# Performance work log

Measured on AMD Instinct MI355X. Metric: run time of the kernel, lower is better.

Reference implementation:

```python
import jax, jax.numpy as jnp
import numpy as np

I, J, B, H = 256, 256, 64, 1024
NHID, NCLS = 1024, 3


def setup_inputs() -> dict:
    key = jax.random.key(0)
    ks = jax.random.split(key, 12)
    inp = {
        "P_enc": jax.random.normal(ks[0], (I, B, H), jnp.float32),
        "H_enc": jax.random.normal(ks[1], (J, B, H), jnp.float32),
        "P_emb": jax.random.normal(ks[2], (I, B, H), jnp.float32),
        "H_emb": jax.random.normal(ks[3], (J, B, H), jnp.float32),
        "prem_mask": jax.random.bernoulli(ks[4], 0.15, (I, B)),
        "hypo_mask": jax.random.bernoulli(ks[5], 0.15, (J, B)),
        # compare MLP: Linear(2H, NHID) -> ReLU -> Linear(NHID, NHID) -> ReLU
        "cW1": jax.random.normal(ks[6], (2 * H, NHID), jnp.float32) * 0.02,
        "cb1": jnp.zeros((NHID,), jnp.float32),
        "cW2": jax.random.normal(ks[7], (NHID, NHID), jnp.float32) * 0.02,
        "cb2": jnp.zeros((NHID,), jnp.float32),
        # agg MLP: Linear(2*NHID, NHID) -> ReLU -> Linear(NHID, NCLS)
        "aW1": jax.random.normal(ks[8], (2 * NHID, NHID), jnp.float32) * 0.02,
        "ab1": jnp.zeros((NHID,), jnp.float32),
        "aW2": jax.random.normal(ks[9], (NHID, NCLS), jnp.float32) * 0.02,
        "ab2": jnp.zeros((NCLS,), jnp.float32),
    }
    return inp


def reference(P_enc, H_enc, P_emb, H_emb, prem_mask, hypo_mask,
              cW1, cb1, cW2, cb2, aW1, ab1, aW2, ab2):
    # Dropout is identity at inference.
    def compare(x):
        h = jax.nn.relu(x @ cW1 + cb1)
        return jax.nn.relu(h @ cW2 + cb2)

    # S[b,i,j] = <P_enc[i,b,:], H_enc[j,b,:]>
    S = jnp.einsum('ibh,jbh->bij', P_enc, H_enc)

    # Premise-side masking on rows i, softmax over premise positions (axis=1)
    S_m = jnp.where(prem_mask.T[:, :, None], -jnp.inf, S)  # [b,i,j]
    P_attn = jax.nn.softmax(S_m, axis=1)
    H_ctx = jnp.einsum('bij,ibh->jbh', P_attn, P_emb)      # [j,b,h]
    H_ctx = jnp.where(hypo_mask[:, :, None], 0.0, H_ctx)
    H_comp = compare(jnp.concatenate([H_emb, H_ctx], axis=-1))  # [j,b,nhid]

    # Hypothesis-side: transpose of the UNMASKED scores
    St = jnp.swapaxes(S, 1, 2)                              # [b,j,i]
    St = jnp.where(hypo_mask.T[:, :, None], -jnp.inf, St)
    H_attn = jax.nn.softmax(St, axis=1)
    P_ctx = jnp.einsum('bji,jbh->ibh', H_attn, H_emb)       # [i,b,h]
    P_ctx = jnp.where(prem_mask[:, :, None], 0.0, P_ctx)
    P_comp = compare(jnp.concatenate([P_emb, P_ctx], axis=-1))  # [i,b,nhid]

    pool = jnp.concatenate([H_comp.sum(axis=0), P_comp.sum(axis=0)], axis=-1)  # [b, 2*nhid]
    out = jax.nn.relu(pool @ aW1 + ab1) @ aW2 + ab2          # [b, ncls]
    return out
```

## Files before the change

### kernel.cpp

```cpp
#include <hip/hip_runtime.h>
#include <cstdint>
#include <cstddef>

typedef unsigned short ushort_t;
typedef unsigned char uchar_t;
typedef __attribute__((ext_vector_type(4))) float f4;
typedef __attribute__((ext_vector_type(4))) unsigned int u4;

#define DEVI static __device__ __forceinline__

DEVI ushort_t f2bf(float x) {
  union { float f; unsigned int u; } v; v.f = x;
  unsigned int r = v.u + 0x7fffu + ((v.u >> 16) & 1u);
  return (ushort_t)(r >> 16);
}
DEVI float bf2f(ushort_t b) {
  union { unsigned int u; float f; } v; v.u = ((unsigned int)b) << 16;
  return v.f;
}
DEVI unsigned pk2(ushort_t a, ushort_t b) { return (unsigned)a | ((unsigned)b << 16); }

DEVI void mfma16(f4& c, u4 a, u4 b) {
  asm("v_mfma_f32_16x16x32_bf16 %0, %1, %2, %0" : "+v"(c) : "v"(a), "v"(b));
}

constexpr int LDR = 40;

__global__ __launch_bounds__(256) void prep_masks_kernel(
    const uchar_t* __restrict__ prem, const uchar_t* __restrict__ hypo,
    uchar_t* __restrict__ premT, uchar_t* __restrict__ hypoT) {
  __shared__ int flagP, flagH;
  int t = threadIdx.x;
  if (t == 0) { flagP = 0; flagH = 0; }
  __syncthreads();
  int locP = 0, locH = 0;
  for (int i = t; i < 16384; i += 256) {
    if (i & 3) { locP |= prem[i]; locH |= hypo[i]; }
  }
  if (locP) atomicOr(&flagP, 1);
  if (locH) atomicOr(&flagH, 1);
  __syncthreads();
  bool p8 = flagP != 0, h8 = flagH != 0;
  for (int i = t; i < 16384; i += 256) {
    int p = i >> 6, b = i & 63;
    premT[b * 256 + p] = p8 ? prem[i] : prem[i * 4];
    hypoT[b * 256 + p] = h8 ? hypo[i] : hypo[i * 4];
  }
}

__global__ __launch_bounds__(256) void transpose_w_kernel(
    const float* __restrict__ Win, ushort_t* __restrict__ Thi,
    ushort_t* __restrict__ Tlo, int N, int K) {
  __shared__ float tl[64][65];
  int k0 = blockIdx.x * 64, n0 = blockIdx.y * 64;
  int t = threadIdx.x;
#pragma unroll
  for (int it = 0; it < 16; ++it) {
    int idx = t + it * 256;
    int k = idx >> 6, n = idx & 63;
    tl[n][k] = Win[(size_t)(k0 + k) * N + n0 + n];
  }
  __syncthreads();
#pragma unroll
  for (int it = 0; it < 16; ++it) {
    int idx = t + it * 256;
    int n = idx >> 6, k = idx & 63;
    float x = tl[n][k];
    ushort_t h = f2bf(x);
    Thi[(size_t)(n0 + n) * K + k0 + k] = h;
    if (Tlo) Tlo[(size_t)(n0 + n) * K + k0 + k] = f2bf(x - bf2f(h));
  }
}

__global__ __launch_bounds__(256) void gemm_s_kernel(
    const float* __restrict__ Penc, const float* __restrict__ Henc,
    float* __restrict__ S) {
  __shared__ ushort_t lAh[128 * LDR], lAl[128 * LDR], lBh[128 * LDR], lBl[128 * LDR];
  const int t = threadIdx.x;
  const int b = blockIdx.z;
  const int i0 = blockIdx.x * 128, j0 = blockIdx.y * 128;
  const float* Ab = Penc + (size_t)i0 * 64 * 1024 + (size_t)b * 1024;
  const float* Bb = Henc + (size_t)j0 * 64 * 1024 + (size_t)b * 1024;
  const int lda = 64 * 1024;
  const int lane = t & 63, wave = t >> 6;
  const int wr = (wave >> 1) << 6, wc = (wave & 1) << 6;
  const int fr = lane & 15, fg = lane >> 4;

  f4 acc[4][4];
#pragma unroll
  for (int m = 0; m < 4; ++m)
#pragma unroll
    for (int n = 0; n < 4; ++n) acc[m][n] = f4{0.f, 0.f, 0.f, 0.f};

  for (int k0 = 0; k0 < 1024; k0 += 32) {
    __syncthreads();
#pragma unroll
    for (int c = 0; c < 2; ++c) {
      int ch = t + (c << 8);
      int row = ch >> 2, kp = (ch & 3) << 3;
      {
        const float* p = Ab + (size_t)row * lda + k0 + kp;
        f4 x0 = *(const f4*)p, x1 = *(const f4*)(p + 4);
        ushort_t hh[8], ll[8];
#pragma unroll
        for (int q = 0; q < 4; ++q) {
          ushort_t h0 = f2bf(x0[q]); hh[q] = h0; ll[q] = f2bf(x0[q] - bf2f(h0));
          ushort_t h1 = f2bf(x1[q]); hh[4 + q] = h1; ll[4 + q] = f2bf(x1[q] - bf2f(h1));
        }
        u4 hv = { pk2(hh[0], hh[1]), pk2(hh[2], hh[3]), pk2(hh[4], hh[5]), pk2(hh[6], hh[7]) };
        u4 lv = { pk2(ll[0], ll[1]), pk2(ll[2], ll[3]), pk2(ll[4], ll[5]), pk2(ll[6], ll[7]) };
        *(u4*)(lAh + row * LDR + kp) = hv;
        *(u4*)(lAl + row * LDR + kp) = lv;
      }
      {
        const float* p = Bb + (size_t)row * lda + k0 + kp;
        f4 x0 = *(const f4*)p, x1 = *(const f4*)(p + 4);
        ushort_t hh[8], ll[8];
#pragma unroll
        for (int q = 0; q < 4; ++q) {
          ushort_t h0 = f2bf(x0[q]); hh[q] = h0; ll[q] = f2bf(x0[q] - bf2f(h0));
          ushort_t h1 = f2bf(x1[q]); hh[4 + q] = h1; ll[4 + q] = f2bf(x1[q] - bf2f(h1));
        }
        u4 hv = { pk2(hh[0], hh[1]), pk2(hh[2], hh[3]), pk2(hh[4], hh[5]), pk2(hh[6], hh[7]) };
        u4 lv = { pk2(ll[0], ll[1]), pk2(ll[2], ll[3]), pk2(ll[4], ll[5]), pk2(ll[6], ll[7]) };
        *(u4*)(lBh + row * LDR + kp) = hv;
        *(u4*)(lBl + row * LDR + kp) = lv;
      }
    }
    __syncthreads();
    u4 ah[4], al[4], bh[4], bl[4];
#pragma unroll
    for (int m = 0; m < 4; ++m) {
      int off = (wr + m * 16 + fr) * LDR + (fg << 3);
      ah[m] = *(const u4*)(lAh + off);
      al[m] = *(const u4*)(lAl + off);
    }
#pragma unroll
    for (int n = 0; n < 4; ++n) {
      int off = (wc + n * 16 + fr) * LDR + (fg << 3);
      bh[n] = *(const u4*)(lBh + off);
      bl[n] = *(const u4*)(lBl + off);
    }
#pragma unroll
    for (int m = 0; m < 4; ++m)
#pragma unroll
      for (int n = 0; n < 4; ++n) {
        mfma16(acc[m][n], ah[m], bh[n]);
        mfma16(acc[m][n], ah[m], bl[n]);
        mfma16(acc[m][n], al[m], bh[n]);
      }
  }

  float* Sb = S + (size_t)b * 256 * 256;
#pragma unroll
  for (int m = 0; m < 4; ++m)
#pragma unroll
    for (int n = 0; n < 4; ++n)
#pragma unroll
      for (int r = 0; r < 4; ++r) {
        int row = i0 + wr + m * 16 + fg * 4 + r;
        int col = j0 + wc + n * 16 + fr;
        Sb[(size_t)row * 256 + col] = acc[m][n][r];
      }
}

__global__ __launch_bounds__(256) void softmax_rows_kernel(
    const float* __restrict__ S, const uchar_t* __restrict__ hypoT,
    ushort_t* __restrict__ W) {
  int r = blockIdx.x * 4 + (threadIdx.x >> 6);
  int lane = threadIdx.x & 63;
  int b = r >> 8;
  const float* row = S + (size_t)r * 256;
  f4 x = *(const f4*)(row + lane * 4);
  const uchar_t* mp = hypoT + b * 256 + lane * 4;
  float v0 = mp[0] ? -1e30f : x[0];
  float v1 = mp[1] ? -1e30f : x[1];
  float v2 = mp[2] ? -1e30f : x[2];
  float v3 = mp[3] ? -1e30f : x[3];
  float m = fmaxf(fmaxf(v0, v1), fmaxf(v2, v3));
#pragma unroll
  for (int off = 32; off > 0; off >>= 1) m = fmaxf(m, __shfl_xor(m, off));
  float e0 = expf(v0 - m), e1 = expf(v1 - m), e2 = expf(v2 - m), e3 = expf(v3 - m);
  float s = e0 + e1 + e2 + e3;
#pragma unroll
  for (int off = 32; off > 0; off >>= 1) s += __shfl_xor(s, off);
  float rinv = 1.0f / s;
  u4 dummy;
  (void)dummy;
  ushort_t w0 = f2bf(e0 * rinv), w1 = f2bf(e1 * rinv), w2 = f2bf(e2 * rinv), w3 = f2bf(e3 * rinv);
  unsigned out0 = pk2(w0, w1), out1 = pk2(w2, w3);
  typedef __attribute__((ext_vector_type(2))) unsigned int u2;
  *(u2*)(W + (size_t)r * 256 + lane * 4) = u2{out0, out1};
}

__global__ __launch_bounds__(256) void softmax_cols_kernel(
    const float* __restrict__ S, const uchar_t* __restrict__ premT,
    ushort_t* __restrict__ V) {
  __shared__ float tl[32][257];
  __shared__ float pm[8][32], ps[8][32], mfin[32], rs[32];
  int t = threadIdx.x;
  int jl = t & 31, ig = t >> 5;
  int b = blockIdx.y, j0 = blockIdx.x * 32;
  const float* Sb = S + (size_t)b * 65536;
  const uchar_t* pmsk = premT + b * 256;
  for (int i = ig; i < 256; i += 8)
    tl[jl][i] = pmsk[i] ? -1e30f : Sb[(size_t)i * 256 + j0 + jl];
  __syncthreads();
  float m = -3e30f;
#pragma unroll 8
  for (int ii = 0; ii < 32; ++ii) m = fmaxf(m, tl[jl][ig * 32 + ii]);
  float s = 0.f;
#pragma unroll 8
  for (int ii = 0; ii < 32; ++ii) s += expf(tl[jl][ig * 32 + ii] - m);
  pm[ig][jl] = m; ps[ig][jl] = s;
  __syncthreads();
  if (t < 32) {
    float M = pm[0][t];
#pragma unroll
    for (int g = 1; g < 8; ++g) M = fmaxf(M, pm[g][t]);
    float ss = 0.f;
#pragma unroll
    for (int g = 0; g < 8; ++g) ss += ps[g][t] * expf(pm[g][t] - M);
    mfin[t] = M; rs[t] = 1.0f / ss;
  }
  __syncthreads();
  for (int j2 = 0; j2 < 32; ++j2) {
    float val = expf(tl[j2][t] - mfin[j2]) * rs[j2];
    V[((size_t)b * 256 + j0 + j2) * 256 + t] = f2bf(val);
  }
}

__global__ __launch_bounds__(256) void transpose_pos_h_kernel(
    const float* __restrict__ E, ushort_t* __restrict__ T) {
  __shared__ ushort_t tl[64][65];
  int i0 = blockIdx.x * 64, h0 = blockIdx.y * 64, b = blockIdx.z;
  int t = threadIdx.x;
#pragma unroll
  for (int it = 0; it < 16; ++it) {
    int idx = t + it * 256;
    int i = idx >> 6, h = idx & 63;
    tl[h][i] = f2bf(E[((size_t)(i0 + i) * 64 + b) * 1024 + h0 + h]);
  }
  __syncthreads();
#pragma unroll
  for (int it = 0; it < 16; ++it) {
    int idx = t + it * 256;
    int h = idx >> 6, i = idx & 63;
    T[((size_t)b * 1024 + h0 + h) * 256 + i0 + i] = tl[h][i];
  }
}

__global__ __launch_bounds__(256) void cast_half_kernel(
    const float* __restrict__ E, ushort_t* __restrict__ X) {
  size_t idx = (size_t)blockIdx.x * 256 + threadIdx.x;
  size_t r = idx >> 7;
  int h8 = ((int)idx & 127) << 3;
  const f4* p = (const f4*)(E + r * 1024 + h8);
  f4 a = p[0], c = p[1];
  ushort_t hh[8];
#pragma unroll
  for (int q = 0; q < 4; ++q) { hh[q] = f2bf(a[q]); hh[4 + q] = f2bf(c[q]); }
  u4 v = { pk2(hh[0], hh[1]), pk2(hh[2], hh[3]), pk2(hh[4], hh[5]), pk2(hh[6], hh[7]) };
  *(u4*)(X + r * 2048 + h8) = v;
}

DEVI void gemm_core(const ushort_t* __restrict__ A, int lda,
                    const ushort_t* __restrict__ B, int ldb, int K,
                    ushort_t* lA, ushort_t* lB, f4 acc[4][4],
                    int t, int wr, int wc, int fr, int fg) {
  for (int k0 = 0; k0 < K; k0 += 32) {
    __syncthreads();
#pragma unroll
    for (int c = 0; c < 2; ++c) {
      int ch = t + (c << 8);
      int row = ch >> 2, kp = (ch & 3) << 3;
      *(u4*)(lA + row * LDR + kp) = *(const u4*)(A + (size_t)row * lda + k0 + kp);
      *(u4*)(lB + row * LDR + kp) = *(const u4*)(B + (size_t)row * ldb + k0 + kp);
    }
    __syncthreads();
    u4 af[4], bfr[4];
#pragma unroll
    for (int m = 0; m < 4; ++m) af[m] = *(const u4*)(lA + (wr + m * 16 + fr) * LDR + (fg << 3));
#pragma unroll
    for (int n = 0; n < 4; ++n) bfr[n] = *(const u4*)(lB + (wc + n * 16 + fr) * LDR + (fg << 3));
#pragma unroll
    for (int m = 0; m < 4; ++m)
#pragma unroll
      for (int n = 0; n < 4; ++n) mfma16(acc[m][n], af[m], bfr[n]);
  }
}

__global__ __launch_bounds__(256) void gemm_ctx_kernel(
    const ushort_t* __restrict__ Attn, const ushort_t* __restrict__ T,
    const uchar_t* __restrict__ maskT, ushort_t* __restrict__ X) {
  __shared__ ushort_t lA[128 * LDR], lB[128 * LDR];
  int t = threadIdx.x;
  int b = blockIdx.z;
  int m0 = blockIdx.x * 128, n0 = blockIdx.y * 128;
  const ushort_t* A = Attn + (size_t)b * 65536 + (size_t)m0 * 256;
  const ushort_t* B = T + (size_t)b * 1024 * 256 + (size_t)n0 * 256;
  int lane = t & 63, wave = t >> 6;
  int wr = (wave >> 1) << 6, wc = (wave & 1) << 6;
  int fr = lane & 15, fg = lane >> 4;
  f4 acc[4][4];
#pragma unroll
  for (int m = 0; m < 4; ++m)
#pragma unroll
    for (int n = 0; n < 4; ++n) acc[m][n] = f4{0.f, 0.f, 0.f, 0.f};
  gemm_core(A, 256, B, 256, 256, lA, lB, acc, t, wr, wc, fr, fg);
#pragma unroll
  for (int m = 0; m < 4; ++m)
#pragma unroll
    for (int n = 0; n < 4; ++n)
#pragma unroll
      for (int r = 0; r < 4; ++r) {
        int gm = m0 + wr + m * 16 + fg * 4 + r;
        int gn = n0 + wc + n * 16 + fr;
        float v = maskT[b * 256 + gm] ? 0.f : acc[m][n][r];
        X[((size_t)gm * 64 + b) * 2048 + 1024 + gn] = f2bf(v);
      }
}

__global__ __launch_bounds__(256) void gemm_mlp_kernel(
    const ushort_t* __restrict__ A, int lda, const ushort_t* __restrict__ W,
    const float* __restrict__ bias, ushort_t* __restrict__ C, int K) {
  __shared__ ushort_t lA[128 * LDR], lB[128 * LDR];
  int t = threadIdx.x;
  int m0 = blockIdx.x * 128, n0 = blockIdx.y * 128;
  int lane = t & 63, wave = t >> 6;
  int wr = (wave >> 1) << 6, wc = (wave & 1) << 6;
  int fr = lane & 15, fg = lane >> 4;
  f4 acc[4][4];
#pragma unroll
  for (int m = 0; m < 4; ++m)
#pragma unroll
    for (int n = 0; n < 4; ++n) acc[m][n] = f4{0.f, 0.f, 0.f, 0.f};
  gemm_core(A + (size_t)m0 * lda, lda, W + (size_t)n0 * K, K, K, lA, lB, acc,
            t, wr, wc, fr, fg);
#pragma unroll
  for (int m = 0; m < 4; ++m)
#pragma unroll
    for (int n = 0; n < 4; ++n)
#pragma unroll
      for (int r = 0; r < 4; ++r) {
        int gm = m0 + wr + m * 16 + fg * 4 + r;
        int gn = n0 + wc + n * 16 + fr;
        float v = acc[m][n][r] + bias[gn];
        v = v > 0.f ? v : 0.f;
        C[(size_t)gm * 1024 + gn] = f2bf(v);
      }
}

__global__ __launch_bounds__(256) void pool_reduce_kernel(
    const ushort_t* __restrict__ H2, float* __restrict__ pool, int coff) {
  int n = blockIdx.x * 256 + threadIdx.x;
  int b = blockIdx.y;
  float s = 0.f;
  for (int j = 0; j < 256; ++j)
    s += bf2f(H2[((size_t)j * 64 + b) * 1024 + n]);
  pool[b * 2048 + coff + n] = s;
}

__global__ __launch_bounds__(256) void pool_split_kernel(
    const float* __restrict__ pool, ushort_t* __restrict__ ph, ushort_t* __restrict__ pl) {
  int i = blockIdx.x * 256 + threadIdx.x;
  float x = pool[i];
  ushort_t h = f2bf(x);
  ph[i] = h;
  pl[i] = f2bf(x - bf2f(h));
}

__global__ __launch_bounds__(256) void gemm_agg1_kernel(
    const ushort_t* __restrict__ Ph, const ushort_t* __restrict__ Pl,
    const ushort_t* __restrict__ Wh, const ushort_t* __restrict__ Wl,
    const float* __restrict__ bias, float* __restrict__ z) {
  __shared__ ushort_t lAh[64 * LDR], lAl[64 * LDR], lBh[128 * LDR], lBl[128 * LDR];
  int t = threadIdx.x;
  int n0 = blockIdx.x * 128;
  int lane = t & 63, wave = t >> 6;
  int wc = wave * 32;
  int fr = lane & 15, fg = lane >> 4;
  f4 acc[4][2];
#pragma unroll
  for (int m = 0; m < 4; ++m)
#pragma unroll
    for (int n = 0; n < 2; ++n) acc[m][n] = f4{0.f, 0.f, 0.f, 0.f};

  for (int k0 = 0; k0 < 2048; k0 += 32) {
    __syncthreads();
    {
      int row = t >> 2, kp = (t & 3) << 3;
      *(u4*)(lAh + row * LDR + kp) = *(const u4*)(Ph + (size_t)row * 2048 + k0 + kp);
      *(u4*)(lAl + row * LDR + kp) = *(const u4*)(Pl + (size_t)row * 2048 + k0 + kp);
    }
#pragma unroll
    for (int c = 0; c < 2; ++c) {
      int ch = t + (c << 8);
      int row = ch >> 2, kp = (ch & 3) << 3;
      *(u4*)(lBh + row * LDR + kp) = *(const u4*)(Wh + (size_t)(n0 + row) * 2048 + k0 + kp);
      *(u4*)(lBl + row * LDR + kp) = *(const u4*)(Wl + (size_t)(n0 + row) * 2048 + k0 + kp);
    }
    __syncthreads();
    u4 ah[4], al[4], bh[2], bl[2];
#pragma unroll
    for (int m = 0; m < 4; ++m) {
      int off = (m * 16 + fr) * LDR + (fg << 3);
      ah[m] = *(const u4*)(lAh + off);
      al[m] = *(const u4*)(lAl + off);
    }
#pragma unroll
    for (int n = 0; n < 2; ++n) {
      int off = (wc + n * 16 + fr) * LDR + (fg << 3);
      bh[n] = *(const u4*)(lBh + off);
      bl[n] = *(const u4*)(lBl + off);
    }
#pragma unroll
    for (int m = 0; m < 4; ++m)
#pragma unroll
      for (int n = 0; n < 2; ++n) {
        mfma16(acc[m][n], ah[m], bh[n]);
        mfma16(acc[m][n], ah[m], bl[n]);
        mfma16(acc[m][n], al[m], bh[n]);
      }
  }
#pragma unroll
  for (int m = 0; m < 4; ++m)
#pragma unroll
    for (int n = 0; n < 2; ++n)
#pragma unroll
      for (int r = 0; r < 4; ++r) {
        int row = m * 16 + fg * 4 + r;
        int col = n0 + wc + n * 16 + fr;
        float v = acc[m][n][r] + bias[col];
        z[row * 1024 + col] = v > 0.f ? v : 0.f;
      }
}

__global__ __launch_bounds__(64) void agg2_kernel(
    const float* __restrict__ z, const float* __restrict__ aW2,
    const float* __restrict__ ab2, float* __restrict__ out) {
  int b = blockIdx.x, lane = threadIdx.x;
  float a0 = 0.f, a1 = 0.f, a2 = 0.f;
  for (int k = lane; k < 1024; k += 64) {
    float zv = z[b * 1024 + k];
    a0 += zv * aW2[k * 3 + 0];
    a1 += zv * aW2[k * 3 + 1];
    a2 += zv * aW2[k * 3 + 2];
  }
#pragma unroll
  for (int off = 32; off > 0; off >>= 1) {
    a0 += __shfl_xor(a0, off);
    a1 += __shfl_xor(a1, off);
    a2 += __shfl_xor(a2, off);
  }
  if (lane == 0) {
    out[b * 3 + 0] = a0 + ab2[0];
    out[b * 3 + 1] = a1 + ab2[1];
    out[b * 3 + 2] = a2 + ab2[2];
  }
}

extern "C" void kernel_launch(void* const* d_in, const int* in_sizes, int n_in,
                              void* d_out, int out_size, void* d_ws, size_t ws_size,
                              hipStream_t stream) {
  const float* P_enc = (const float*)d_in[0];
  const float* H_enc = (const float*)d_in[1];
  const float* P_emb = (const float*)d_in[2];
  const float* H_emb = (const float*)d_in[3];
  const uchar_t* prem = (const uchar_t*)d_in[4];
  const uchar_t* hypo = (const uchar_t*)d_in[5];
  const float* cW1 = (const float*)d_in[6];
  const float* cb1 = (const float*)d_in[7];
  const float* cW2 = (const float*)d_in[8];
  const float* cb2 = (const float*)d_in[9];
  const float* aW1 = (const float*)d_in[10];
  const float* ab1 = (const float*)d_in[11];
  const float* aW2 = (const float*)d_in[12];
  const float* ab2 = (const float*)d_in[13];

  char* w = (char*)d_ws;
  auto alloc = [&](size_t bytes) { char* p = w; w += bytes; return p; };
  float* S        = (float*)alloc(16777216);
  ushort_t* Wsm   = (ushort_t*)alloc(8388608);
  ushort_t* Vsm   = (ushort_t*)alloc(8388608);
  ushort_t* Tbuf  = (ushort_t*)alloc(33554432);
  ushort_t* X     = (ushort_t*)alloc(67108864);
  ushort_t* H1    = (ushort_t*)alloc(33554432);
  ushort_t* H2    = (ushort_t*)alloc(33554432);
  ushort_t* cW1T  = (ushort_t*)alloc(4194304);
  ushort_t* cW2T  = (ushort_t*)alloc(2097152);
  ushort_t* aW1Th = (ushort_t*)alloc(4194304);
  ushort_t* aW1Tl = (ushort_t*)alloc(4194304);
  float* pool     = (float*)alloc(524288);
  ushort_t* poolh = (ushort_t*)alloc(262144);
  ushort_t* pooll = (ushort_t*)alloc(262144);
  float* z        = (float*)alloc(262144);
  uchar_t* premT  = (uchar_t*)alloc(16384);
  uchar_t* hypoT  = (uchar_t*)alloc(16384);

  prep_masks_kernel<<<1, 256, 0, stream>>>(prem, hypo, premT, hypoT);
  transpose_w_kernel<<<dim3(32, 16), 256, 0, stream>>>(cW1, cW1T, (ushort_t*)nullptr, 1024, 2048);
  transpose_w_kernel<<<dim3(16, 16), 256, 0, stream>>>(cW2, cW2T, (ushort_t*)nullptr, 1024, 1024);
  transpose_w_kernel<<<dim3(32, 16), 256, 0, stream>>>(aW1, aW1Th, aW1Tl, 1024, 2048);

  gemm_s_kernel<<<dim3(2, 2, 64), 256, 0, stream>>>(P_enc, H_enc, S);
  softmax_rows_kernel<<<4096, 256, 0, stream>>>(S, hypoT, Wsm);
  softmax_cols_kernel<<<dim3(8, 64), 256, 0, stream>>>(S, premT, Vsm);

  transpose_pos_h_kernel<<<dim3(4, 16, 64), 256, 0, stream>>>(P_emb, Tbuf);
  cast_half_kernel<<<8192, 256, 0, stream>>>(H_emb, X);
  gemm_ctx_kernel<<<dim3(2, 8, 64), 256, 0, stream>>>(Vsm, Tbuf, hypoT, X);
  gemm_mlp_kernel<<<dim3(128, 8), 256, 0, stream>>>(X, 2048, cW1T, cb1, H1, 2048);
  gemm_mlp_kernel<<<dim3(128, 8), 256, 0, stream>>>(H1, 1024, cW2T, cb2, H2, 1024);
  pool_reduce_kernel<<<dim3(4, 64), 256, 0, stream>>>(H2, pool, 0);

  transpose_pos_h_kernel<<<dim3(4, 16, 64), 256, 0, stream>>>(H_emb, Tbuf);
  cast_half_kernel<<<8192, 256, 0, stream>>>(P_emb, X);
  gemm_ctx_kernel<<<dim3(2, 8, 64), 256, 0, stream>>>(Wsm, Tbuf, premT, X);
  gemm_mlp_kernel<<<dim3(128, 8), 256, 0, stream>>>(X, 2048, cW1T, cb1, H1, 2048);
  gemm_mlp_kernel<<<dim3(128, 8), 256, 0, stream>>>(H1, 1024, cW2T, cb2, H2, 1024);
  pool_reduce_kernel<<<dim3(4, 64), 256, 0, stream>>>(H2, pool, 1024);

  pool_split_kernel<<<512, 256, 0, stream>>>(pool, poolh, pooll);
  gemm_agg1_kernel<<<8, 256, 0, stream>>>(poolh, pooll, aW1Th, aW1Tl, ab1, z);
  agg2_kernel<<<64, 64, 0, stream>>>(z, aW2, ab2, (float*)d_out);
}
```

Measured before the change: 707.6 us.

## Fuse embedding cast into MLP GEMM, use direct-to-LDS loads, shrink S tiles

Removes the cast_half kernel by having the first MLP GEMM read fp32 embeddings and convert them to bf16 while staging its A tile, writing the context half to a separate buffer. GEMM tile staging switches to global_load_lds (direct global-to-LDS 16-byte loads) where the builtin exists, with unpadded 32-wide LDS rows. The S GEMM moves to 64x64 tiles to launch more blocks, and pool reduction is split into partial and final kernels for more parallelism. Unpadded LDS rows may cause bank conflicts, and the fused fp32 loads add per-block conversion work.

```diff
diff --git a/kernel.cpp b/kernel.cpp
--- a/kernel.cpp
+++ b/kernel.cpp
@@ -6,6 +6,7 @@
 typedef unsigned char uchar_t;
 typedef __attribute__((ext_vector_type(4))) float f4;
 typedef __attribute__((ext_vector_type(4))) unsigned int u4;
+typedef __attribute__((ext_vector_type(2))) unsigned int u2;
 
 #define DEVI static __device__ __forceinline__
 
@@ -25,6 +26,54 @@
 }
 
 constexpr int LDR = 40;
+
+#if defined(__has_builtin)
+#if __has_builtin(__builtin_amdgcn_global_load_lds)
+#define HAS_GLD 1
+#endif
+#endif
+#ifndef HAS_GLD
+#define HAS_GLD 0
+#endif
+
+#if HAS_GLD
+typedef const __attribute__((address_space(1))) unsigned int* gas1_t;
+typedef __attribute__((address_space(3))) unsigned int* las3_t;
+DEVI void gld16(const void* g, void* l) {
+  __builtin_amdgcn_global_load_lds((gas1_t)g, (las3_t)l, 16, 0, 0);
+}
+#endif
+
+DEVI void stage_tile(const ushort_t* __restrict__ src, int srcStride, int k0,
+                     ushort_t* lT, int t) {
+#if HAS_GLD
+  int w = t >> 6, lane = t & 63;
+#pragma unroll
+  for (int c = 0; c < 2; ++c) {
+    int row = c * 64 + w * 16 + (lane >> 2);
+    const ushort_t* g = src + (size_t)row * srcStride + k0 + (lane & 3) * 8;
+    gld16(g, lT + (c * 64 + w * 16) * 32);
+  }
+#else
+  int row = t >> 1, kp = (t & 1) << 4;
+  const ushort_t* g = src + (size_t)row * srcStride + k0 + kp;
+  *(u4*)(lT + row * 32 + kp) = *(const u4*)g;
+  *(u4*)(lT + row * 32 + kp + 8) = *(const u4*)(g + 8);
+#endif
+}
+
+DEVI void compute16(const ushort_t* lA, const ushort_t* lB, f4 acc[4][4],
+                    int wr, int wc, int fr, int fg) {
+  u4 af[4], bfv[4];
+#pragma unroll
+  for (int m = 0; m < 4; ++m) af[m] = *(const u4*)(lA + (wr + m * 16 + fr) * 32 + (fg << 3));
+#pragma unroll
+  for (int n = 0; n < 4; ++n) bfv[n] = *(const u4*)(lB + (wc + n * 16 + fr) * 32 + (fg << 3));
+#pragma unroll
+  for (int m = 0; m < 4; ++m)
+#pragma unroll
+    for (int n = 0; n < 4; ++n) mfma16(acc[m][n], af[m], bfv[n]);
+}
 
 __global__ __launch_bounds__(256) void prep_masks_kernel(
     const uchar_t* __restrict__ prem, const uchar_t* __restrict__ hypo,
@@ -75,92 +124,84 @@
 __global__ __launch_bounds__(256) void gemm_s_kernel(
     const float* __restrict__ Penc, const float* __restrict__ Henc,
     float* __restrict__ S) {
-  __shared__ ushort_t lAh[128 * LDR], lAl[128 * LDR], lBh[128 * LDR], lBl[128 * LDR];
+  __shared__ ushort_t lAh[64 * LDR], lAl[64 * LDR], lBh[64 * LDR], lBl[64 * LDR];
   const int t = threadIdx.x;
   const int b = blockIdx.z;
-  const int i0 = blockIdx.x * 128, j0 = blockIdx.y * 128;
-  const float* Ab = Penc + (size_t)i0 * 64 * 1024 + (size_t)b * 1024;
-  const float* Bb = Henc + (size_t)j0 * 64 * 1024 + (size_t)b * 1024;
+  const int i0 = blockIdx.x * 64, j0 = blockIdx.y * 64;
   const int lda = 64 * 1024;
+  const float* Ab = Penc + (size_t)i0 * lda + (size_t)b * 1024;
+  const float* Bb = Henc + (size_t)j0 * lda + (size_t)b * 1024;
   const int lane = t & 63, wave = t >> 6;
-  const int wr = (wave >> 1) << 6, wc = (wave & 1) << 6;
+  const int wr = (wave >> 1) << 5, wc = (wave & 1) << 5;
   const int fr = lane & 15, fg = lane >> 4;
 
-  f4 acc[4][4];
-#pragma unroll
-  for (int m = 0; m < 4; ++m)
-#pragma unroll
-    for (int n = 0; n < 4; ++n) acc[m][n] = f4{0.f, 0.f, 0.f, 0.f};
-
+  f4 acc[2][2];
+#pragma unroll
+  for (int m = 0; m < 2; ++m)
+#pragma unroll
+    for (int n = 0; n < 2; ++n) acc[m][n] = f4{0.f, 0.f, 0.f, 0.f};
+
+  const int row = t >> 2, kp = (t & 3) << 3;
   for (int k0 = 0; k0 < 1024; k0 += 32) {
-    __syncthreads();
-#pragma unroll
-    for (int c = 0; c < 2; ++c) {
-      int ch = t + (c << 8);
-      int row = ch >> 2, kp = (ch & 3) << 3;
-      {
-        const float* p = Ab + (size_t)row * lda + k0 + kp;
-        f4 x0 = *(const f4*)p, x1 = *(const f4*)(p + 4);
-        ushort_t hh[8], ll[8];
-#pragma unroll
-        for (int q = 0; q < 4; ++q) {
-          ushort_t h0 = f2bf(x0[q]); hh[q] = h0; ll[q] = f2bf(x0[q] - bf2f(h0));
-          ushort_t h1 = f2bf(x1[q]); hh[4 + q] = h1; ll[4 + q] = f2bf(x1[q] - bf2f(h1));
-        }
-        u4 hv = { pk2(hh[0], hh[1]), pk2(hh[2], hh[3]), pk2(hh[4], hh[5]), pk2(hh[6], hh[7]) };
-        u4 lv = { pk2(ll[0], ll[1]), pk2(ll[2], ll[3]), pk2(ll[4], ll[5]), pk2(ll[6], ll[7]) };
-        *(u4*)(lAh + row * LDR + kp) = hv;
-        *(u4*)(lAl + row * LDR + kp) = lv;
-      }
-      {
-        const float* p = Bb + (size_t)row * lda + k0 + kp;
-        f4 x0 = *(const f4*)p, x1 = *(const f4*)(p + 4);
-        ushort_t hh[8], ll[8];
-#pragma unroll
-        for (int q = 0; q < 4; ++q) {
-          ushort_t h0 = f2bf(x0[q]); hh[q] = h0; ll[q] = f2bf(x0[q] - bf2f(h0));
-          ushort_t h1 = f2bf(x1[q]); hh[4 + q] = h1; ll[4 + q] = f2bf(x1[q] - bf2f(h1));
-        }
-        u4 hv = { pk2(hh[0], hh[1]), pk2(hh[2], hh[3]), pk2(hh[4], hh[5]), pk2(hh[6], hh[7]) };
-        u4 lv = { pk2(ll[0], ll[1]), pk2(ll[2], ll[3]), pk2(ll[4], ll[5]), pk2(ll[6], ll[7]) };
-        *(u4*)(lBh + row * LDR + kp) = hv;
-        *(u4*)(lBl + row * LDR + kp) = lv;
-      }
-    }
-    __syncthreads();
-    u4 ah[4], al[4], bh[4], bl[4];
-#pragma unroll
-    for (int m = 0; m < 4; ++m) {
+    {
+      const float* p = Ab + (size_t)row * lda + k0 + kp;
+      f4 x0 = *(const f4*)p, x1 = *(const f4*)(p + 4);
+      ushort_t hh[8], ll[8];
+#pragma unroll
+      for (int q = 0; q < 4; ++q) {
+        ushort_t h0 = f2bf(x0[q]); hh[q] = h0; ll[q] = f2bf(x0[q] - bf2f(h0));
+        ushort_t h1 = f2bf(x1[q]); hh[4 + q] = h1; ll[4 + q] = f2bf(x1[q] - bf2f(h1));
+      }
+      *(u4*)(lAh + row * LDR + kp) = u4{ pk2(hh[0], hh[1]), pk2(hh[2], hh[3]), pk2(hh[4], hh[5]), pk2(hh[6], hh[7]) };
+      *(u4*)(lAl + row * LDR + kp) = u4{ pk2(ll[0], ll[1]), pk2(ll[2], ll[3]), pk2(ll[4], ll[5]), pk2(ll[6], ll[7]) };
+    }
+    {
+      const float* p = Bb + (size_t)row * lda + k0 + kp;
+      f4 x0 = *(const f4*)p, x1 = *(const f4*)(p + 4);
+      ushort_t hh[8], ll[8];
+#pragma unroll
+      for (int q = 0; q < 4; ++q) {
+        ushort_t h0 = f2bf(x0[q]); hh[q] = h0; ll[q] = f2bf(x0[q] - bf2f(h0));
+        ushort_t h1 = f2bf(x1[q]); hh[4 + q] = h1; ll[4 + q] = f2bf(x1[q] - bf2f(h1));
+      }
+      *(u4*)(lBh + row * LDR + kp) = u4{ pk2(hh[0], hh[1]), pk2(hh[2], hh[3]), pk2(hh[4], hh[5]), pk2(hh[6], hh[7]) };
+      *(u4*)(lBl + row * LDR + kp) = u4{ pk2(ll[0], ll[1]), pk2(ll[2], ll[3]), pk2(ll[4], ll[5]), pk2(ll[6], ll[7]) };
+    }
+    __syncthreads();
+    u4 ah[2], al[2], bh[2], bl[2];
+#pragma unroll
+    for (int m = 0; m < 2; ++m) {
       int off = (wr + m * 16 + fr) * LDR + (fg << 3);
       ah[m] = *(const u4*)(lAh + off);
       al[m] = *(const u4*)(lAl + off);
     }
 #pragma unroll
-    for (int n = 0; n < 4; ++n) {
+    for (int n = 0; n < 2; ++n) {
       int off = (wc + n * 16 + fr) * LDR + (fg << 3);
       bh[n] = *(const u4*)(lBh + off);
       bl[n] = *(const u4*)(lBl + off);
     }
 #pragma unroll
-    for (int m = 0; m < 4; ++m)
-#pragma unroll
-      for (int n = 0; n < 4; ++n) {
+    for (int m = 0; m < 2; ++m)
+#pragma unroll
+      for (int n = 0; n < 2; ++n) {
         mfma16(acc[m][n], ah[m], bh[n]);
         mfma16(acc[m][n], ah[m], bl[n]);
         mfma16(acc[m][n], al[m], bh[n]);
       }
-  }
-
-  float* Sb = S + (size_t)b * 256 * 256;
-#pragma unroll
-  for (int m = 0; m < 4; ++m)
-#pragma unroll
-    for (int n = 0; n < 4; ++n)
+    __syncthreads();
+  }
+
+  float* Sb = S + (size_t)b * 65536;
+#pragma unroll
+  for (int m = 0; m < 2; ++m)
+#pragma unroll
+    for (int n = 0; n < 2; ++n)
 #pragma unroll
       for (int r = 0; r < 4; ++r) {
-        int row = i0 + wr + m * 16 + fg * 4 + r;
+        int rrow = i0 + wr + m * 16 + fg * 4 + r;
         int col = j0 + wc + n * 16 + fr;
-        Sb[(size_t)row * 256 + col] = acc[m][n][r];
+        Sb[(size_t)rrow * 256 + col] = acc[m][n][r];
       }
 }
 
@@ -185,12 +226,8 @@
 #pragma unroll
   for (int off = 32; off > 0; off >>= 1) s += __shfl_xor(s, off);
   float rinv = 1.0f / s;
-  u4 dummy;
-  (void)dummy;
   ushort_t w0 = f2bf(e0 * rinv), w1 = f2bf(e1 * rinv), w2 = f2bf(e2 * rinv), w3 = f2bf(e3 * rinv);
-  unsigned out0 = pk2(w0, w1), out1 = pk2(w2, w3);
-  typedef __attribute__((ext_vector_type(2))) unsigned int u2;
-  *(u2*)(W + (size_t)r * 256 + lane * 4) = u2{out0, out1};
+  *(u2*)(W + (size_t)r * 256 + lane * 4) = u2{ pk2(w0, w1), pk2(w2, w3) };
 }
 
 __global__ __launch_bounds__(256) void softmax_cols_kernel(
@@ -250,55 +287,15 @@
   }
 }
 
-__global__ __launch_bounds__(256) void cast_half_kernel(
-    const float* __restrict__ E, ushort_t* __restrict__ X) {
-  size_t idx = (size_t)blockIdx.x * 256 + threadIdx.x;
-  size_t r = idx >> 7;
-  int h8 = ((int)idx & 127) << 3;
-  const f4* p = (const f4*)(E + r * 1024 + h8);
-  f4 a = p[0], c = p[1];
-  ushort_t hh[8];
-#pragma unroll
-  for (int q = 0; q < 4; ++q) { hh[q] = f2bf(a[q]); hh[4 + q] = f2bf(c[q]); }
-  u4 v = { pk2(hh[0], hh[1]), pk2(hh[2], hh[3]), pk2(hh[4], hh[5]), pk2(hh[6], hh[7]) };
-  *(u4*)(X + r * 2048 + h8) = v;
-}
-
-DEVI void gemm_core(const ushort_t* __restrict__ A, int lda,
-                    const ushort_t* __restrict__ B, int ldb, int K,
-                    ushort_t* lA, ushort_t* lB, f4 acc[4][4],
-                    int t, int wr, int wc, int fr, int fg) {
-  for (int k0 = 0; k0 < K; k0 += 32) {
-    __syncthreads();
-#pragma unroll
-    for (int c = 0; c < 2; ++c) {
-      int ch = t + (c << 8);
-      int row = ch >> 2, kp = (ch & 3) << 3;
-      *(u4*)(lA + row * LDR + kp) = *(const u4*)(A + (size_t)row * lda + k0 + kp);
-      *(u4*)(lB + row * LDR + kp) = *(const u4*)(B + (size_t)row * ldb + k0 + kp);
-    }
-    __syncthreads();
-    u4 af[4], bfr[4];
-#pragma unroll
-    for (int m = 0; m < 4; ++m) af[m] = *(const u4*)(lA + (wr + m * 16 + fr) * LDR + (fg << 3));
-#pragma unroll
-    for (int n = 0; n < 4; ++n) bfr[n] = *(const u4*)(lB + (wc + n * 16 + fr) * LDR + (fg << 3));
-#pragma unroll
-    for (int m = 0; m < 4; ++m)
-#pragma unroll
-      for (int n = 0; n < 4; ++n) mfma16(acc[m][n], af[m], bfr[n]);
-  }
-}
-
 __global__ __launch_bounds__(256) void gemm_ctx_kernel(
     const ushort_t* __restrict__ Attn, const ushort_t* __restrict__ T,
-    const uchar_t* __restrict__ maskT, ushort_t* __restrict__ X) {
-  __shared__ ushort_t lA[128 * LDR], lB[128 * LDR];
+    const uchar_t* __restrict__ maskT, ushort_t* __restrict__ Xc) {
+  __shared__ ushort_t lA[128 * 32], lB[128 * 32];
   int t = threadIdx.x;
   int b = blockIdx.z;
   int m0 = blockIdx.x * 128, n0 = blockIdx.y * 128;
   const ushort_t* A = Attn + (size_t)b * 65536 + (size_t)m0 * 256;
-  const ushort_t* B = T + (size_t)b * 1024 * 256 + (size_t)n0 * 256;
+  const ushort_t* B = T + (size_t)b * 262144 + (size_t)n0 * 256;
   int lane = t & 63, wave = t >> 6;
   int wr = (wave >> 1) << 6, wc = (wave & 1) << 6;
   int fr = lane & 15, fg = lane >> 4;
@@ -307,7 +304,13 @@
   for (int m = 0; m < 4; ++m)
 #pragma unroll
     for (int n = 0; n < 4; ++n) acc[m][n] = f4{0.f, 0.f, 0.f, 0.f};
-  gemm_core(A, 256, B, 256, 256, lA, lB, acc, t, wr, wc, fr, fg);
+  for (int k0 = 0; k0 < 256; k0 += 32) {
+    stage_tile(A, 256, k0, lA, t);
+    stage_tile(B, 256, k0, lB, t);
+    __syncthreads();
+    compute16(lA, lB, acc, wr, wc, fr, fg);
+    __syncthreads();
+  }
 #pragma unroll
   for (int m = 0; m < 4; ++m)
 #pragma unroll
@@ -317,14 +320,15 @@
         int gm = m0 + wr + m * 16 + fg * 4 + r;
         int gn = n0 + wc + n * 16 + fr;
         float v = maskT[b * 256 + gm] ? 0.f : acc[m][n][r];
-        X[((size_t)gm * 64 + b) * 2048 + 1024 + gn] = f2bf(v);
+        Xc[((size_t)gm * 64 + b) * 1024 + gn] = f2bf(v);
       }
 }
 
 __global__ __launch_bounds__(256) void gemm_mlp_kernel(
-    const ushort_t* __restrict__ A, int lda, const ushort_t* __restrict__ W,
-    const float* __restrict__ bias, ushort_t* __restrict__ C, int K) {
-  __shared__ ushort_t lA[128 * LDR], lB[128 * LDR];
+    const float* __restrict__ Ef, const ushort_t* __restrict__ Actx,
+    const ushort_t* __restrict__ W, int ldw, const float* __restrict__ bias,
+    ushort_t* __restrict__ C, int Kb) {
+  __shared__ ushort_t lA[128 * 32], lB[128 * 32];
   int t = threadIdx.x;
   int m0 = blockIdx.x * 128, n0 = blockIdx.y * 128;
   int lane = t & 63, wave = t >> 6;
@@ -335,8 +339,40 @@
   for (int m = 0; m < 4; ++m)
 #pragma unroll
     for (int n = 0; n < 4; ++n) acc[m][n] = f4{0.f, 0.f, 0.f, 0.f};
-  gemm_core(A + (size_t)m0 * lda, lda, W + (size_t)n0 * K, K, K, lA, lB, acc,
-            t, wr, wc, fr, fg);
+
+  const ushort_t* Wn = W + (size_t)n0 * ldw;
+  if (Ef) {
+    int row = t >> 1, kp = (t & 1) << 4;
+    for (int k0 = 0; k0 < 1024; k0 += 32) {
+      const float* p = Ef + (size_t)(m0 + row) * 1024 + k0 + kp;
+      f4 x0 = *(const f4*)p, x1 = *(const f4*)(p + 4);
+      f4 x2 = *(const f4*)(p + 8), x3 = *(const f4*)(p + 12);
+      ushort_t hh[16];
+#pragma unroll
+      for (int q = 0; q < 4; ++q) {
+        hh[q] = f2bf(x0[q]); hh[4 + q] = f2bf(x1[q]);
+        hh[8 + q] = f2bf(x2[q]); hh[12 + q] = f2bf(x3[q]);
+      }
+      *(u4*)(lA + row * 32 + kp) =
+          u4{ pk2(hh[0], hh[1]), pk2(hh[2], hh[3]), pk2(hh[4], hh[5]), pk2(hh[6], hh[7]) };
+      *(u4*)(lA + row * 32 + kp + 8) =
+          u4{ pk2(hh[8], hh[9]), pk2(hh[10], hh[11]), pk2(hh[12], hh[13]), pk2(hh[14], hh[15]) };
+      stage_tile(Wn, ldw, k0, lB, t);
+      __syncthreads();
+      compute16(lA, lB, acc, wr, wc, fr, fg);
+      __syncthreads();
+    }
+  }
+  const ushort_t* Abase = Actx + (size_t)m0 * Kb;
+  const int wkoff = Ef ? 1024 : 0;
+  for (int k0 = 0; k0 < Kb; k0 += 32) {
+    stage_tile(Abase, Kb, k0, lA, t);
+    stage_tile(Wn, ldw, wkoff + k0, lB, t);
+    __syncthreads();
+    compute16(lA, lB, acc, wr, wc, fr, fg);
+    __syncthreads();
+  }
+
 #pragma unroll
   for (int m = 0; m < 4; ++m)
 #pragma unroll
@@ -351,23 +387,31 @@
       }
 }
 
-__global__ __launch_bounds__(256) void pool_reduce_kernel(
-    const ushort_t* __restrict__ H2, float* __restrict__ pool, int coff) {
-  int n = blockIdx.x * 256 + threadIdx.x;
-  int b = blockIdx.y;
+__global__ __launch_bounds__(256) void pool_partial_kernel(
+    const ushort_t* __restrict__ H2, float* __restrict__ partial, int coff) {
+  int jc = blockIdx.x, b = blockIdx.y, t = threadIdx.x;
+  float a0 = 0.f, a1 = 0.f, a2 = 0.f, a3 = 0.f;
+  for (int j = jc * 32; j < jc * 32 + 32; ++j) {
+    u2 v = *(const u2*)(H2 + ((size_t)(j * 64 + b)) * 1024 + t * 4);
+    a0 += bf2f((ushort_t)(v[0] & 0xffff));
+    a1 += bf2f((ushort_t)(v[0] >> 16));
+    a2 += bf2f((ushort_t)(v[1] & 0xffff));
+    a3 += bf2f((ushort_t)(v[1] >> 16));
+  }
+  *(f4*)(partial + ((size_t)(jc * 64 + b)) * 2048 + coff + t * 4) = f4{a0, a1, a2, a3};
+}
+
+__global__ __launch_bounds__(256) void pool_final_kernel(
+    const float* __restrict__ partial, ushort_t* __restrict__ ph,
+    ushort_t* __restrict__ pl) {
+  int idx = blockIdx.x * 256 + threadIdx.x;
+  int b = idx >> 11, k = idx & 2047;
   float s = 0.f;
-  for (int j = 0; j < 256; ++j)
-    s += bf2f(H2[((size_t)j * 64 + b) * 1024 + n]);
-  pool[b * 2048 + coff + n] = s;
-}
-
-__global__ __launch_bounds__(256) void pool_split_kernel(
-    const float* __restrict__ pool, ushort_t* __restrict__ ph, ushort_t* __restrict__ pl) {
-  int i = blockIdx.x * 256 + threadIdx.x;
-  float x = pool[i];
-  ushort_t h = f2bf(x);
-  ph[i] = h;
-  pl[i] = f2bf(x - bf2f(h));
+#pragma unroll
+  for (int jc = 0; jc < 8; ++jc) s += partial[((size_t)(jc * 64 + b)) * 2048 + k];
+  ushort_t h = f2bf(s);
+  ph[idx] = h;
+  pl[idx] = f2bf(s - bf2f(h));
 }
 
 __global__ __launch_bounds__(256) void gemm_agg1_kernel(
@@ -483,15 +527,15 @@
   float* S        = (float*)alloc(16777216);
   ushort_t* Wsm   = (ushort_t*)alloc(8388608);
   ushort_t* Vsm   = (ushort_t*)alloc(8388608);
-  ushort_t* Tbuf  = (ushort_t*)alloc(33554432);
-  ushort_t* X     = (ushort_t*)alloc(67108864);
+  ushort_t* T     = (ushort_t*)alloc(33554432);
+  ushort_t* Xc    = (ushort_t*)alloc(33554432);
   ushort_t* H1    = (ushort_t*)alloc(33554432);
   ushort_t* H2    = (ushort_t*)alloc(33554432);
   ushort_t* cW1T  = (ushort_t*)alloc(4194304);
   ushort_t* cW2T  = (ushort_t*)alloc(2097152);
   ushort_t* aW1Th = (ushort_t*)alloc(4194304);
   ushort_t* aW1Tl = (ushort_t*)alloc(4194304);
-  float* pool     = (float*)alloc(524288);
+  float* partial  = (float*)alloc(4194304);
   ushort_t* poolh = (ushort_t*)alloc(262144);
   ushort_t* pooll = (ushort_t*)alloc(262144);
   float* z        = (float*)alloc(262144);
@@ -503,25 +547,23 @@
   transpose_w_kernel<<<dim3(16, 16), 256, 0, stream>>>(cW2, cW2T, (ushort_t*)nullptr, 1024, 1024);
   transpose_w_kernel<<<dim3(32, 16), 256, 0, stream>>>(aW1, aW1Th, aW1Tl, 1024, 2048);
 
-  gemm_s_kernel<<<dim3(2, 2, 64), 256, 0, stream>>>(P_enc, H_enc, S);
+  gemm_s_kernel<<<dim3(4, 4, 64), 256, 0, stream>>>(P_enc, H_enc, S);
   softmax_rows_kernel<<<4096, 256, 0, stream>>>(S, hypoT, Wsm);
   softmax_cols_kernel<<<dim3(8, 64), 256, 0, stream>>>(S, premT, Vsm);
 
-  transpose_pos_h_kernel<<<dim3(4, 16, 64), 256, 0, stream>>>(P_emb, Tbuf);
-  cast_half_kernel<<<8192, 256, 0, stream>>>(H_emb, X);
-  gemm_ctx_kernel<<<dim3(2, 8, 64), 256, 0, stream>>>(Vsm, Tbuf, hypoT, X);
-  gemm_mlp_kernel<<<dim3(128, 8), 256, 0, stream>>>(X, 2048, cW1T, cb1, H1, 2048);
-  gemm_mlp_kernel<<<dim3(128, 8), 256, 0, stream>>>(H1, 1024, cW2T, cb2, H2, 1024);
-  pool_reduce_kernel<<<dim3(4, 64), 256, 0, stream>>>(H2, pool, 0);
-
-  transpose_pos_h_kernel<<<dim3(4, 16, 64), 256, 0, stream>>>(H_emb, Tbuf);
-  cast_half_kernel<<<8192, 256, 0, stream>>>(P_emb, X);
-  gemm_ctx_kernel<<<dim3(2, 8, 64), 256, 0, stream>>>(Wsm, Tbuf, premT, X);
-  gemm_mlp_kernel<<<dim3(128, 8), 256, 0, stream>>>(X, 2048, cW1T, cb1, H1, 2048);
-  gemm_mlp_kernel<<<dim3(128, 8), 256, 0, stream>>>(H1, 1024, cW2T, cb2, H2, 1024);
-  pool_reduce_kernel<<<dim3(4, 64), 256, 0, stream>>>(H2, pool, 1024);
-
-  pool_split_kernel<<<512, 256, 0, stream>>>(pool, poolh, pooll);
+  transpose_pos_h_kernel<<<dim3(4, 16, 64), 256, 0, stream>>>(P_emb, T);
+  gemm_ctx_kernel<<<dim3(2, 8, 64), 256, 0, stream>>>(Vsm, T, hypoT, Xc);
+  gemm_mlp_kernel<<<dim3(128, 8), 256, 0, stream>>>(H_emb, Xc, cW1T, 2048, cb1, H1, 1024);
+  gemm_mlp_kernel<<<dim3(128, 8), 256, 0, stream>>>(nullptr, H1, cW2T, 1024, cb2, H2, 1024);
+  pool_partial_kernel<<<dim3(8, 64), 256, 0, stream>>>(H2, partial, 0);
+
+  transpose_pos_h_kernel<<<dim3(4, 16, 64), 256, 0, stream>>>(H_emb, T);
+  gemm_ctx_kernel<<<dim3(2, 8, 64), 256, 0, stream>>>(Wsm, T, premT, Xc);
+  gemm_mlp_kernel<<<dim3(128, 8), 256, 0, stream>>>(P_emb, Xc, cW1T, 2048, cb1, H1, 1024);
+  gemm_mlp_kernel<<<dim3(128, 8), 256, 0, stream>>>(nullptr, H1, cW2T, 1024, cb2, H2, 1024);
+  pool_partial_kernel<<<dim3(8, 64), 256, 0, stream>>>(H2, partial, 1024);
+
+  pool_final_kernel<<<512, 256, 0, stream>>>(partial, poolh, pooll);
   gemm_agg1_kernel<<<8, 256, 0, stream>>>(poolh, pooll, aW1Th, aW1Tl, ab1, z);
   agg2_kernel<<<64, 64, 0, stream>>>(z, aW2, ab2, (float*)d_out);
 }
```

New measurement: 640.2 us. -9.5%, faster.
